# Optimization experiments

Measured on AMD Instinct MI355X. Metric: run time of the kernel, lower is better.

Reference implementation:

```python
import jax, jax.numpy as jnp
import numpy as np

B, N, E = 32, 128, 16384
D, H, O, A = 72, 72, 72, 4   # n_input, n_hidden, n_output, n_node_attr
C_WEIGHT = 1.0
EPS = 1e-5  # BatchNorm1d default eps


def setup_inputs() -> dict:
    key = jax.random.key(0)
    ks = jax.random.split(key, 16)
    rn = lambda k, shp, s=0.05: jax.random.normal(k, shp, jnp.float32) * s
    return {
        "h": jax.random.normal(ks[0], (B, N, D), jnp.float32),
        "x": jax.random.normal(ks[1], (B, N, 4), jnp.float32),
        "edgei": jax.random.randint(ks[2], (B, E), 0, N),
        "edgej": jax.random.randint(ks[3], (B, E), 0, N),
        "node_attr": jax.random.normal(ks[4], (B, N, A), jnp.float32),
        # phi_e: Linear(2D+2 -> H, no bias), BN, ReLU, Linear(H->H), ReLU
        "We1": rn(ks[5], (2 * D + 2, H)),
        "g1": jnp.ones((H,), jnp.float32), "b1": jnp.zeros((H,), jnp.float32),
        "We2": rn(ks[6], (H, H)), "be2": jnp.zeros((H,), jnp.float32),
        # phi_m: Linear(H->1), Sigmoid
        "Wm": rn(ks[7], (H, 1)), "bm": jnp.zeros((1,), jnp.float32),
        # phi_x: Linear(H->H), ReLU, Linear(H->1, no bias, tiny init)
        "Wx1": rn(ks[8], (H, H)), "bx1": jnp.zeros((H,), jnp.float32),
        "Wx2": rn(ks[9], (H, 1), 0.001),
        # phi_h: Linear(H+D+A -> H), BN, ReLU, Linear(H->O)
        "Wh1": rn(ks[10], (H + D + A, H)), "bh1": jnp.zeros((H,), jnp.float32),
        "gh": jnp.ones((H,), jnp.float32), "bh": jnp.zeros((H,), jnp.float32),
        "Wh2": rn(ks[11], (H, O)), "bh2": jnp.zeros((O,), jnp.float32),
    }


def _psi(p):
    return jnp.sign(p) * jnp.log1p(jnp.abs(p))


def _normsq4(p):  # Minkowski norm: p0^2 - p1^2 - p2^2 - p3^2
    psq = p * p
    return 2.0 * psq[..., 0] - psq.sum(axis=-1)


def _dotsq4(p, q):  # Minkowski inner product
    pq = p * q
    return 2.0 * pq[..., 0] - pq.sum(axis=-1)


def _batchnorm(z, g, b):  # training-mode BatchNorm1d over flattened batch dim
    mu = z.mean(axis=0)
    var = z.var(axis=0)
    return (z - mu) * jax.lax.rsqrt(var + EPS) * g + b


_seg_sum = jax.vmap(lambda d, s: jax.ops.segment_sum(d, s, num_segments=N))


def reference(h, x, edgei, edgej, node_attr,
              We1, g1, b1, We2, be2, Wm, bm,
              Wx1, bx1, Wx2, Wh1, bh1, gh, bh, Wh2, bh2):
    # gather edge endpoint features (equiv. to torch.gather along dim 1)
    xi = jnp.take_along_axis(x, edgei[:, :, None], axis=1)    # [B,E,4]
    xj = jnp.take_along_axis(x, edgej[:, :, None], axis=1)
    hi = jnp.take_along_axis(h, edgei[:, :, None], axis=1)    # [B,E,D]
    hj = jnp.take_along_axis(h, edgej[:, :, None], axis=1)
    x_diff = xi - xj
    norms = _psi(_normsq4(x_diff))[..., None]                 # [B,E,1]
    dots = _psi(_dotsq4(xi, xj))[..., None]                   # [B,E,1]

    # m_model: phi_e then sigmoid gate phi_m
    feat = jnp.concatenate([hi, hj, norms, dots], axis=-1)    # [B,E,2D+2]
    z = feat.reshape(-1, 2 * D + 2) @ We1
    z = jax.nn.relu(_batchnorm(z, g1, b1))
    z = jax.nn.relu(z @ We2 + be2)
    m = z.reshape(B, E, H)
    m = m * jax.nn.sigmoid(m @ Wm + bm)                       # gated messages

    # x_model: equivariant coordinate update (segment mean over edges)
    gate = jax.nn.relu(m @ Wx1 + bx1) @ Wx2                   # [B,E,1]
    trans = jnp.clip(x_diff * gate, -100.0, 100.0)
    agg = _seg_sum(trans, edgei)                              # [B,N,4]
    cnt = _seg_sum(jnp.ones_like(trans), edgei)
    x_out = x + (agg / jnp.maximum(cnt, 1.0)) * C_WEIGHT

    # h_model: segment sum of messages, node MLP, residual
    magg = _seg_sum(m, edgei)                                 # [B,N,H]
    hin = jnp.concatenate([h, magg, node_attr], axis=-1).reshape(-1, H + D + A)
    z2 = hin @ Wh1 + bh1
    z2 = jax.nn.relu(_batchnorm(z2, gh, bh))
    z2 = z2 @ Wh2 + bh2
    h_out = h + z2.reshape(B, N, O)

    return (h_out, x_out, m)
```

## Files before the change

kernel.cpp:

```cpp
#include <hip/hip_runtime.h>

#define BB 32
#define NN 128
#define EE 16384
#define ROWS_E (BB*EE)
#define ROWS_N (BB*NN)
#define EPS_BN 1e-5f

#define XOUT_OFF (ROWS_N*72)
#define M_OFF    (XOUT_OFF + ROWS_N*4)

#define ST1_OFF 0
#define ST2_OFF 512
#define AGG_OFF 1024
#define CNT_OFF (AGG_OFF + ROWS_N*4)
#define MAGG_OFF (CNT_OFF + ROWS_N)
#define Z2_OFF (MAGG_OFF + ROWS_N*72)
#define ZERO_FLOATS Z2_OFF
#define WB_OFF (Z2_OFF + ROWS_N*72)

#define WE1T_OFF 0
#define WE2T_OFF 13440
#define WX1T_OFF 21760
#define WH1T_OFF 30080
#define WH2T_OFF 43520
#define WB_TOTAL 51840

typedef __attribute__((ext_vector_type(8))) short short8;
typedef __attribute__((ext_vector_type(4))) float f32x4;

__device__ __forceinline__ float psi_f(float p) {
    return copysignf(log1pf(fabsf(p)), p);
}
__device__ __forceinline__ unsigned short f2bf(float f) {
    union { float f; unsigned u; } v; v.f = f;
    unsigned r = v.u + 0x7fffu + ((v.u >> 16) & 1u);
    return (unsigned short)(r >> 16);
}
__device__ __forceinline__ unsigned pk(float a, float b) {
    return (unsigned)f2bf(a) | ((unsigned)f2bf(b) << 16);
}

__global__ void k_prep(const float* __restrict__ We1, const float* __restrict__ We2,
                       const float* __restrict__ Wx1, const float* __restrict__ Wh1,
                       const float* __restrict__ Wh2, unsigned short* __restrict__ wb)
{
    int idx = blockIdx.x * 256 + threadIdx.x;
    if (idx >= WB_TOTAL) return;
    const float* src; int off, n, k, K;
    if (idx < WE2T_OFF)      { off = idx;            n = off/168; k = off%168; src = We1; K = 146; }
    else if (idx < WH1T_OFF && idx >= WX1T_OFF) { off = idx - WX1T_OFF; n = off/104; k = off%104; src = Wx1; K = 72; }
    else if (idx < WX1T_OFF) { off = idx - WE2T_OFF; n = off/104; k = off%104; src = We2; K = 72; }
    else if (idx < WH2T_OFF) { off = idx - WH1T_OFF; n = off/168; k = off%168; src = Wh1; K = 148; }
    else                     { off = idx - WH2T_OFF; n = off/104; k = off%104; src = Wh2; K = 72; }
    float v = (n < 72 && k < K) ? src[k * 72 + n] : 0.f;
    wb[idx] = f2bf(v);
}

__device__ __forceinline__ void stage_feat(
    unsigned short* At, const float* __restrict__ h, const float* __restrict__ x,
    const int* __restrict__ ei, const int* __restrict__ ej, int tid, int blk)
{
    int rl = tid >> 1, half = tid & 1;
    int row = blk * 128 + rl;
    int b = row >> 14;
    int i = ei[row], j = ej[row];
    int node = half ? j : i;
    const float4* hp = (const float4*)(h + (size_t)(b * 128 + node) * 72);
    uint2* arow = (uint2*)(&At[rl * 160 + half * 72]);
    #pragma unroll
    for (int q = 0; q < 18; q++) {
        float4 v = hp[q];
        arow[q] = make_uint2(pk(v.x, v.y), pk(v.z, v.w));
    }
    if (half == 0) {
        float4 xi = *(const float4*)(x + (size_t)(b * 128 + i) * 4);
        float4 xj = *(const float4*)(x + (size_t)(b * 128 + j) * 4);
        float d0 = xi.x - xj.x, d1 = xi.y - xj.y, d2 = xi.z - xj.z, d3 = xi.w - xj.w;
        float nrm = d0*d0 - d1*d1 - d2*d2 - d3*d3;
        float dot = xi.x*xj.x - xi.y*xj.y - xi.z*xj.z - xi.w*xj.w;
        *(unsigned*)(&At[rl * 160 + 144]) = pk(psi_f(nrm), psi_f(dot));
        unsigned* tp = (unsigned*)(&At[rl * 160 + 146]);
        tp[0] = 0u; tp[1] = 0u; tp[2] = 0u;
    } else {
        unsigned* tp = (unsigned*)(&At[rl * 160 + 152]);
        tp[0] = 0u; tp[1] = 0u; tp[2] = 0u; tp[3] = 0u;
    }
}

__global__ __launch_bounds__(256, 4) void k_edge_stats(
    const float* __restrict__ h, const float* __restrict__ x,
    const int* __restrict__ ei, const int* __restrict__ ej,
    const unsigned short* __restrict__ We1t, float* __restrict__ st)
{
    __shared__ unsigned short At[128 * 160];
    int tid = threadIdx.x;
    stage_feat(At, h, x, ei, ej, tid, blockIdx.x);

    int wv = tid >> 6, lane = tid & 63, c = lane & 15, quad = lane >> 4;
    f32x4 acc[2][5] = {};
    for (int kc = 0; kc < 5; kc++) {
        int k0 = kc * 32 + quad * 8;
        short8 a0 = *(const short8*)(&At[(wv * 32 + c) * 160 + k0]);
        short8 a1 = *(const short8*)(&At[(wv * 32 + 16 + c) * 160 + k0]);
        #pragma unroll
        for (int ct = 0; ct < 5; ct++) {
            short8 bf = *(const short8*)(&We1t[(ct * 16 + c) * 168 + k0]);
            acc[0][ct] = __builtin_amdgcn_mfma_f32_16x16x32_bf16(a0, bf, acc[0][ct], 0, 0, 0);
            acc[1][ct] = __builtin_amdgcn_mfma_f32_16x16x32_bf16(a1, bf, acc[1][ct], 0, 0, 0);
        }
    }
    float* sredw = (float*)(&At[wv * 32 * 160]);
    #pragma unroll
    for (int ct = 0; ct < 5; ct++) {
        int col = ct * 16 + c;
        float s = 0.f, q = 0.f;
        #pragma unroll
        for (int rt = 0; rt < 2; rt++)
            #pragma unroll
            for (int r = 0; r < 4; r++) {
                float v = acc[rt][ct][r];
                s += v; q += v * v;
            }
        s += __shfl_xor(s, 16); s += __shfl_xor(s, 32);
        q += __shfl_xor(q, 16); q += __shfl_xor(q, 32);
        if (lane < 16 && col < 72) { sredw[col] = s; sredw[72 + col] = q; }
    }
    __syncthreads();
    if (tid < 144) {
        const float* a = (const float*)At;
        atomicAdd(&st[tid], a[tid] + a[2560 + tid] + a[5120 + tid] + a[7680 + tid]);
    }
}

__global__ void k_finalize(float* __restrict__ st, float inv_rows)
{
    int c = threadIdx.x;
    if (c < 72) {
        float mean = st[c] * inv_rows;
        float var  = st[72 + c] * inv_rows - mean * mean;
        st[144 + c] = mean;
        st[216 + c] = rsqrtf(var + EPS_BN);
    }
}

__global__ __launch_bounds__(256, 4) void k_edge_fused(
    const float* __restrict__ h, const float* __restrict__ x,
    const int* __restrict__ ei, const int* __restrict__ ej,
    const float* __restrict__ st1, const float* __restrict__ g1, const float* __restrict__ b1,
    const float* __restrict__ be2, const float* __restrict__ Wm, const float* __restrict__ bm,
    const float* __restrict__ bx1, const float* __restrict__ Wx2,
    const unsigned short* __restrict__ We1t, const unsigned short* __restrict__ We2t,
    const unsigned short* __restrict__ Wx1t,
    float* __restrict__ m, float* __restrict__ agg, float* __restrict__ cnt)
{
    __shared__ unsigned short At[128 * 160];
    int tid = threadIdx.x;
    stage_feat(At, h, x, ei, ej, tid, blockIdx.x);

    int wv = tid >> 6, lane = tid & 63, c = lane & 15, quad = lane >> 4;
    f32x4 acc1[2][5] = {};
    for (int kc = 0; kc < 5; kc++) {
        int k0 = kc * 32 + quad * 8;
        short8 a0 = *(const short8*)(&At[(wv * 32 + c) * 160 + k0]);
        short8 a1 = *(const short8*)(&At[(wv * 32 + 16 + c) * 160 + k0]);
        #pragma unroll
        for (int ct = 0; ct < 5; ct++) {
            short8 bf = *(const short8*)(&We1t[(ct * 16 + c) * 168 + k0]);
            acc1[0][ct] = __builtin_amdgcn_mfma_f32_16x16x32_bf16(a0, bf, acc1[0][ct], 0, 0, 0);
            acc1[1][ct] = __builtin_amdgcn_mfma_f32_16x16x32_bf16(a1, bf, acc1[1][ct], 0, 0, 0);
        }
    }
    const float* mean = st1 + 144;
    const float* inv  = st1 + 216;
    #pragma unroll
    for (int ct = 0; ct < 5; ct++) {
        int col = ct * 16 + c;
        float mu = 0.f, iv = 0.f, ga = 0.f, be = 0.f;
        if (col < 72) { mu = mean[col]; iv = inv[col]; ga = g1[col]; be = b1[col]; }
        #pragma unroll
        for (int rt = 0; rt < 2; rt++)
            #pragma unroll
            for (int r = 0; r < 4; r++) {
                float a = (col < 72) ? fmaxf((acc1[rt][ct][r] - mu) * iv * ga + be, 0.f) : 0.f;
                int lrow = wv * 32 + rt * 16 + quad * 4 + r;
                At[lrow * 160 + col] = f2bf(a);
            }
    }
    {
        int r_ = lane >> 1, h_ = lane & 1;
        uint* zp = (uint*)&At[(wv * 32 + r_) * 160 + 80 + h_ * 8];
        zp[0] = 0u; zp[1] = 0u; zp[2] = 0u; zp[3] = 0u;
    }
    f32x4 acc2[2][5] = {};
    for (int kc = 0; kc < 3; kc++) {
        int k0 = kc * 32 + quad * 8;
        short8 a0 = *(const short8*)(&At[(wv * 32 + c) * 160 + k0]);
        short8 a1 = *(const short8*)(&At[(wv * 32 + 16 + c) * 160 + k0]);
        #pragma unroll
        for (int ct = 0; ct < 5; ct++) {
            short8 bf = *(const short8*)(&We2t[(ct * 16 + c) * 104 + k0]);
            acc2[0][ct] = __builtin_amdgcn_mfma_f32_16x16x32_bf16(a0, bf, acc2[0][ct], 0, 0, 0);
            acc2[1][ct] = __builtin_amdgcn_mfma_f32_16x16x32_bf16(a1, bf, acc2[1][ct], 0, 0, 0);
        }
    }
    float part[2][4] = {};
    float bm0 = bm[0];
    #pragma unroll
    for (int ct = 0; ct < 5; ct++) {
        int col = ct * 16 + c;
        float bias = (col < 72) ? be2[col] : 0.f;
        float wm   = (col < 72) ? Wm[col]  : 0.f;
        #pragma unroll
        for (int rt = 0; rt < 2; rt++)
            #pragma unroll
            for (int r = 0; r < 4; r++) {
                float t = fmaxf(acc2[rt][ct][r] + bias, 0.f);
                acc2[rt][ct][r] = t;
                part[rt][r] += t * wm;
            }
    }
    float sg[2][4];
    #pragma unroll
    for (int rt = 0; rt < 2; rt++)
        #pragma unroll
        for (int r = 0; r < 4; r++) {
            float s = part[rt][r];
            s += __shfl_xor(s, 1); s += __shfl_xor(s, 2);
            s += __shfl_xor(s, 4); s += __shfl_xor(s, 8);
            sg[rt][r] = 1.f / (1.f + expf(-(s + bm0)));
        }
    size_t rbase = (size_t)blockIdx.x * 128 + wv * 32 + quad * 4;
    #pragma unroll
    for (int rt = 0; rt < 2; rt++)
        #pragma unroll
        for (int ct = 0; ct < 5; ct++) {
            int col = ct * 16 + c;
            #pragma unroll
            for (int r = 0; r < 4; r++) {
                float mv = acc2[rt][ct][r] * sg[rt][r];
                int lrow = wv * 32 + rt * 16 + quad * 4 + r;
                At[lrow * 160 + col] = f2bf(mv);
                if (col < 72) m[(rbase + rt * 16 + r) * 72 + col] = mv;
            }
        }
    f32x4 acc3[2][5] = {};
    for (int kc = 0; kc < 3; kc++) {
        int k0 = kc * 32 + quad * 8;
        short8 a0 = *(const short8*)(&At[(wv * 32 + c) * 160 + k0]);
        short8 a1 = *(const short8*)(&At[(wv * 32 + 16 + c) * 160 + k0]);
        #pragma unroll
        for (int ct = 0; ct < 5; ct++) {
            short8 bf = *(const short8*)(&Wx1t[(ct * 16 + c) * 104 + k0]);
            acc3[0][ct] = __builtin_amdgcn_mfma_f32_16x16x32_bf16(a0, bf, acc3[0][ct], 0, 0, 0);
            acc3[1][ct] = __builtin_amdgcn_mfma_f32_16x16x32_bf16(a1, bf, acc3[1][ct], 0, 0, 0);
        }
    }
    float part3[2][4] = {};
    #pragma unroll
    for (int ct = 0; ct < 5; ct++) {
        int col = ct * 16 + c;
        float bias = (col < 72) ? bx1[col] : 0.f;
        float wx   = (col < 72) ? Wx2[col] : 0.f;
        #pragma unroll
        for (int rt = 0; rt < 2; rt++)
            #pragma unroll
            for (int r = 0; r < 4; r++)
                part3[rt][r] += fmaxf(acc3[rt][ct][r] + bias, 0.f) * wx;
    }
    float* gp = (float*)&At[(wv * 32) * 160 + 96];
    #pragma unroll
    for (int rt = 0; rt < 2; rt++)
        #pragma unroll
        for (int r = 0; r < 4; r++) {
            float s = part3[rt][r];
            s += __shfl_xor(s, 1); s += __shfl_xor(s, 2);
            s += __shfl_xor(s, 4); s += __shfl_xor(s, 8);
            if (c == 0) gp[rt * 16 + quad * 4 + r] = s;
        }
    __syncthreads();
    if (tid < 128) {
        size_t erow = (size_t)blockIdx.x * 128 + tid;
        int b = (int)(erow >> 14);
        int i2 = ei[erow], j2 = ej[erow];
        float g2 = *((float*)&At[((tid >> 5) * 32) * 160 + 96] + (tid & 31));
        float4 xi = *(const float4*)(x + (size_t)(b * 128 + i2) * 4);
        float4 xj = *(const float4*)(x + (size_t)(b * 128 + j2) * 4);
        float t0 = fminf(fmaxf((xi.x - xj.x) * g2, -100.f), 100.f);
        float t1 = fminf(fmaxf((xi.y - xj.y) * g2, -100.f), 100.f);
        float t2 = fminf(fmaxf((xi.z - xj.z) * g2, -100.f), 100.f);
        float t3 = fminf(fmaxf((xi.w - xj.w) * g2, -100.f), 100.f);
        float* ap = agg + (size_t)(b * 128 + i2) * 4;
        atomicAdd(ap + 0, t0); atomicAdd(ap + 1, t1);
        atomicAdd(ap + 2, t2); atomicAdd(ap + 3, t3);
        atomicAdd(cnt + (size_t)(b * 128 + i2), 1.f);
    }
}

__global__ __launch_bounds__(256, 4) void k_magg(
    const float* __restrict__ m, const int* __restrict__ ei, float* __restrict__ magg)
{
    __shared__ float accum[128 * 72];
    int tid = threadIdx.x;
    for (int q = tid; q < 9216; q += 256) accum[q] = 0.f;
    __syncthreads();
    int b = blockIdx.x >> 3, chunk = blockIdx.x & 7;
    int wv = tid >> 6, lane = tid & 63;
    int ebase = b * 16384 + chunk * 2048;
    for (int e = wv; e < 2048; e += 4) {
        int erow = ebase + e;
        int node = ei[erow];
        const float* mr = m + (size_t)erow * 72;
        atomicAdd(&accum[node * 72 + lane], mr[lane]);
        if (lane < 8) atomicAdd(&accum[node * 72 + 64 + lane], mr[64 + lane]);
    }
    __syncthreads();
    float* mg = magg + (size_t)b * 9216;
    for (int q = tid; q < 9216; q += 256) atomicAdd(&mg[q], accum[q]);
}

__global__ __launch_bounds__(256) void k_node_gemm1(
    const float* __restrict__ h, const float* __restrict__ node_attr,
    const float* __restrict__ magg, const unsigned short* __restrict__ Wh1t,
    const float* __restrict__ bh1, float* __restrict__ z2, float* __restrict__ st)
{
    __shared__ unsigned short At[128 * 168];
    __shared__ unsigned short Wt[80 * 168];
    __shared__ float sred[4][144];
    int tid = threadIdx.x;
    {
        const uint4* s = (const uint4*)Wh1t; uint4* d = (uint4*)Wt;
        for (int q = tid; q < 1680; q += 256) d[q] = s[q];
    }
    int rl = tid >> 1, half = tid & 1;
    size_t row = (size_t)blockIdx.x * 128 + rl;
    const float4* sp = (const float4*)((half ? magg : h) + row * 72);
    uint2* arow = (uint2*)(&At[rl * 168 + half * 72]);
    #pragma unroll
    for (int q = 0; q < 18; q++) {
        float4 v = sp[q];
        arow[q] = make_uint2(pk(v.x, v.y), pk(v.z, v.w));
    }
    if (half) {
        float4 na = *(const float4*)(node_attr + row * 4);
        *(unsigned*)(&At[rl * 168 + 144]) = pk(na.x, na.y);
        *(unsigned*)(&At[rl * 168 + 146]) = pk(na.z, na.w);
        unsigned* tailp = (unsigned*)(&At[rl * 168 + 148]);
        #pragma unroll
        for (int q = 0; q < 10; q++) tailp[q] = 0u;
    }
    __syncthreads();

    int wv = tid >> 6, lane = tid & 63, c = lane & 15, quad = lane >> 4;
    f32x4 acc[2][5] = {};
    for (int kc = 0; kc < 5; kc++) {
        int k0 = kc * 32 + quad * 8;
        short8 a0 = *(const short8*)(&At[(wv * 32 + c) * 168 + k0]);
        short8 a1 = *(const short8*)(&At[(wv * 32 + 16 + c) * 168 + k0]);
        #pragma unroll
        for (int ct = 0; ct < 5; ct++) {
            short8 bf = *(const short8*)(&Wt[(ct * 16 + c) * 168 + k0]);
            acc[0][ct] = __builtin_amdgcn_mfma_f32_16x16x32_bf16(a0, bf, acc[0][ct], 0, 0, 0);
            acc[1][ct] = __builtin_amdgcn_mfma_f32_16x16x32_bf16(a1, bf, acc[1][ct], 0, 0, 0);
        }
    }
    size_t rbase = (size_t)blockIdx.x * 128 + wv * 32 + quad * 4;
    #pragma unroll
    for (int ct = 0; ct < 5; ct++) {
        int col = ct * 16 + c;
        float bias = (col < 72) ? bh1[col] : 0.f;
        float s = 0.f, q = 0.f;
        #pragma unroll
        for (int rt = 0; rt < 2; rt++) {
            float* op = z2 + (rbase + rt * 16) * 72 + col;
            #pragma unroll
            for (int r = 0; r < 4; r++) {
                float v = acc[rt][ct][r] + bias;
                if (col < 72) op[(size_t)r * 72] = v;
                s += v; q += v * v;
            }
        }
        s += __shfl_xor(s, 16); s += __shfl_xor(s, 32);
        q += __shfl_xor(q, 16); q += __shfl_xor(q, 32);
        if (lane < 16 && col < 72) { sred[wv][col] = s; sred[wv][72 + col] = q; }
    }
    __syncthreads();
    if (tid < 144)
        atomicAdd(&st[tid], sred[0][tid] + sred[1][tid] + sred[2][tid] + sred[3][tid]);
}

__global__ __launch_bounds__(256) void k_node_final(
    const float* __restrict__ h, const float* __restrict__ x,
    const float* __restrict__ z2, const float* __restrict__ st2,
    const float* __restrict__ gh, const float* __restrict__ bh,
    const unsigned short* __restrict__ Wh2t, const float* __restrict__ bh2,
    const float* __restrict__ agg, const float* __restrict__ cnt,
    float* __restrict__ hout, float* __restrict__ xout)
{
    __shared__ unsigned short Zt[128 * 104];
    __shared__ unsigned short Wt[80 * 104];
    int tid = threadIdx.x;
    {
        const uint4* s = (const uint4*)Wh2t; uint4* d = (uint4*)Wt;
        for (int q = tid; q < 1040; q += 256) d[q] = s[q];
    }
    int rl = tid >> 1, half = tid & 1;
    size_t row = (size_t)blockIdx.x * 128 + rl;
    const float* mean = st2 + 144;
    const float* inv  = st2 + 216;
    const float4* zp = (const float4*)(z2 + row * 72) + half * 9;
    uint2* arow = (uint2*)(&Zt[rl * 104 + half * 36]);
    #pragma unroll
    for (int q = 0; q < 9; q++) {
        int k = half * 36 + q * 4;
        float4 v = zp[q];
        float a0 = fmaxf((v.x - mean[k  ]) * inv[k  ] * gh[k  ] + bh[k  ], 0.f);
        float a1 = fmaxf((v.y - mean[k+1]) * inv[k+1] * gh[k+1] + bh[k+1], 0.f);
        float a2 = fmaxf((v.z - mean[k+2]) * inv[k+2] * gh[k+2] + bh[k+2], 0.f);
        float a3 = fmaxf((v.w - mean[k+3]) * inv[k+3] * gh[k+3] + bh[k+3], 0.f);
        arow[q] = make_uint2(pk(a0, a1), pk(a2, a3));
    }
    uint2* prow = (uint2*)(&Zt[rl * 104]);
    #pragma unroll
    for (int q = 0; q < 4; q++) prow[18 + half * 4 + q] = make_uint2(0u, 0u);
    __syncthreads();

    int wv = tid >> 6, lane = tid & 63, c = lane & 15, quad = lane >> 4;
    f32x4 acc[2][5] = {};
    for (int kc = 0; kc < 3; kc++) {
        int k0 = kc * 32 + quad * 8;
        short8 a0 = *(const short8*)(&Zt[(wv * 32 + c) * 104 + k0]);
        short8 a1 = *(const short8*)(&Zt[(wv * 32 + 16 + c) * 104 + k0]);
        #pragma unroll
        for (int ct = 0; ct < 5; ct++) {
            short8 bf = *(const short8*)(&Wt[(ct * 16 + c) * 104 + k0]);
            acc[0][ct] = __builtin_amdgcn_mfma_f32_16x16x32_bf16(a0, bf, acc[0][ct], 0, 0, 0);
            acc[1][ct] = __builtin_amdgcn_mfma_f32_16x16x32_bf16(a1, bf, acc[1][ct], 0, 0, 0);
        }
    }
    size_t rbase = (size_t)blockIdx.x * 128 + wv * 32 + quad * 4;
    #pragma unroll
    for (int rt = 0; rt < 2; rt++)
        #pragma unroll
        for (int ct = 0; ct < 5; ct++) {
            int col = ct * 16 + c;
            if (col < 72) {
                float bias = bh2[col];
                #pragma unroll
                for (int r = 0; r < 4; r++) {
                    size_t gr = (rbase + rt * 16 + r);
                    hout[gr * 72 + col] = h[gr * 72 + col] + acc[rt][ct][r] + bias;
                }
            }
        }
    if (tid < 128) {
        size_t nrow = (size_t)blockIdx.x * 128 + tid;
        float cn = fmaxf(cnt[nrow], 1.f);
        float4 ag = *(const float4*)(agg + nrow * 4);
        float4 xv = *(const float4*)(x + nrow * 4);
        ((float4*)xout)[nrow] = make_float4(xv.x + ag.x / cn, xv.y + ag.y / cn,
                                            xv.z + ag.z / cn, xv.w + ag.w / cn);
    }
}

extern "C" void kernel_launch(void* const* d_in, const int* in_sizes, int n_in,
                              void* d_out, int out_size, void* d_ws, size_t ws_size,
                              hipStream_t stream)
{
    const float* h   = (const float*)d_in[0];
    const float* x   = (const float*)d_in[1];
    const int*   ei  = (const int*)d_in[2];
    const int*   ej  = (const int*)d_in[3];
    const float* na  = (const float*)d_in[4];
    const float* We1 = (const float*)d_in[5];
    const float* g1  = (const float*)d_in[6];
    const float* b1  = (const float*)d_in[7];
    const float* We2 = (const float*)d_in[8];
    const float* be2 = (const float*)d_in[9];
    const float* Wm  = (const float*)d_in[10];
    const float* bm  = (const float*)d_in[11];
    const float* Wx1 = (const float*)d_in[12];
    const float* bx1 = (const float*)d_in[13];
    const float* Wx2 = (const float*)d_in[14];
    const float* Wh1 = (const float*)d_in[15];
    const float* bh1 = (const float*)d_in[16];
    const float* gh  = (const float*)d_in[17];
    const float* bhp = (const float*)d_in[18];
    const float* Wh2 = (const float*)d_in[19];
    const float* bh2 = (const float*)d_in[20];

    float* out  = (float*)d_out;
    float* hout = out;
    float* xout = out + XOUT_OFF;
    float* m    = out + M_OFF;
    float* ws   = (float*)d_ws;
    float* st1  = ws + ST1_OFF;
    float* st2  = ws + ST2_OFF;
    float* agg  = ws + AGG_OFF;
    float* cnt  = ws + CNT_OFF;
    float* magg = ws + MAGG_OFF;
    float* z2   = ws + Z2_OFF;
    unsigned short* wb = (unsigned short*)(ws + WB_OFF);

    hipMemsetAsync(d_ws, 0, (size_t)ZERO_FLOATS * sizeof(float), stream);
    k_prep<<<(WB_TOTAL + 255) / 256, 256, 0, stream>>>(We1, We2, Wx1, Wh1, Wh2, wb);
    k_edge_stats<<<ROWS_E / 128, 256, 0, stream>>>(h, x, ei, ej, wb + WE1T_OFF, st1);
    k_finalize<<<1, 128, 0, stream>>>(st1, 1.0f / (float)ROWS_E);
    k_edge_fused<<<ROWS_E / 128, 256, 0, stream>>>(h, x, ei, ej, st1, g1, b1, be2, Wm, bm,
                                                   bx1, Wx2, wb + WE1T_OFF, wb + WE2T_OFF,
                                                   wb + WX1T_OFF, m, agg, cnt);
    k_magg<<<256, 256, 0, stream>>>(m, ei, magg);
    k_node_gemm1<<<ROWS_N / 128, 256, 0, stream>>>(h, na, magg, wb + WH1T_OFF, bh1, z2, st2);
    k_finalize<<<1, 128, 0, stream>>>(st2, 1.0f / (float)ROWS_N);
    k_node_final<<<ROWS_N / 128, 256, 0, stream>>>(h, x, z2, st2, gh, bhp,
                                                   wb + WH2T_OFF, bh2, agg, cnt, hout, xout);
}
```

Before: 680.1 us.

## Fuse message segment-sum into edge kernel via global atomics, pad LDS rows

Removes the separate k_magg kernel. The edge kernel now atomically adds each gated message value directly into the global per-node aggregate, which avoids re-reading the m tensor from memory. The LDS row stride changes from 160 to 168 to reduce bank conflicts, and launch bounds drop from 4 to 3 blocks per SM. The cost is many more global float atomics on only 128 nodes per batch, which can contend heavily, and fewer resident blocks.

After: 766.0 us. 1.13x slower.

```diff
diff --git a/kernel.cpp b/kernel.cpp
--- a/kernel.cpp
+++ b/kernel.cpp
@@ -25,6 +25,8 @@
 #define WH1T_OFF 30080
 #define WH2T_OFF 43520
 #define WB_TOTAL 51840
+
+#define SS 168
 
 typedef __attribute__((ext_vector_type(8))) short short8;
 typedef __attribute__((ext_vector_type(4))) float f32x4;
@@ -67,7 +69,7 @@
     int i = ei[row], j = ej[row];
     int node = half ? j : i;
     const float4* hp = (const float4*)(h + (size_t)(b * 128 + node) * 72);
-    uint2* arow = (uint2*)(&At[rl * 160 + half * 72]);
+    uint2* arow = (uint2*)(&At[rl * SS + half * 72]);
     #pragma unroll
     for (int q = 0; q < 18; q++) {
         float4 v = hp[q];
@@ -79,21 +81,21 @@
         float d0 = xi.x - xj.x, d1 = xi.y - xj.y, d2 = xi.z - xj.z, d3 = xi.w - xj.w;
         float nrm = d0*d0 - d1*d1 - d2*d2 - d3*d3;
         float dot = xi.x*xj.x - xi.y*xj.y - xi.z*xj.z - xi.w*xj.w;
-        *(unsigned*)(&At[rl * 160 + 144]) = pk(psi_f(nrm), psi_f(dot));
-        unsigned* tp = (unsigned*)(&At[rl * 160 + 146]);
+        *(unsigned*)(&At[rl * SS + 144]) = pk(psi_f(nrm), psi_f(dot));
+        unsigned* tp = (unsigned*)(&At[rl * SS + 146]);
         tp[0] = 0u; tp[1] = 0u; tp[2] = 0u;
     } else {
-        unsigned* tp = (unsigned*)(&At[rl * 160 + 152]);
+        unsigned* tp = (unsigned*)(&At[rl * SS + 152]);
         tp[0] = 0u; tp[1] = 0u; tp[2] = 0u; tp[3] = 0u;
     }
 }
 
-__global__ __launch_bounds__(256, 4) void k_edge_stats(
+__global__ __launch_bounds__(256, 3) void k_edge_stats(
     const float* __restrict__ h, const float* __restrict__ x,
     const int* __restrict__ ei, const int* __restrict__ ej,
     const unsigned short* __restrict__ We1t, float* __restrict__ st)
 {
-    __shared__ unsigned short At[128 * 160];
+    __shared__ unsigned short At[128 * SS];
     int tid = threadIdx.x;
     stage_feat(At, h, x, ei, ej, tid, blockIdx.x);
 
@@ -101,8 +103,8 @@
     f32x4 acc[2][5] = {};
     for (int kc = 0; kc < 5; kc++) {
         int k0 = kc * 32 + quad * 8;
-        short8 a0 = *(const short8*)(&At[(wv * 32 + c) * 160 + k0]);
-        short8 a1 = *(const short8*)(&At[(wv * 32 + 16 + c) * 160 + k0]);
+        short8 a0 = *(const short8*)(&At[(wv * 32 + c) * SS + k0]);
+        short8 a1 = *(const short8*)(&At[(wv * 32 + 16 + c) * SS + k0]);
         #pragma unroll
         for (int ct = 0; ct < 5; ct++) {
             short8 bf = *(const short8*)(&We1t[(ct * 16 + c) * 168 + k0]);
@@ -110,7 +112,7 @@
             acc[1][ct] = __builtin_amdgcn_mfma_f32_16x16x32_bf16(a1, bf, acc[1][ct], 0, 0, 0);
         }
     }
-    float* sredw = (float*)(&At[wv * 32 * 160]);
+    float* sredw = (float*)(&At[wv * 32 * SS]);
     #pragma unroll
     for (int ct = 0; ct < 5; ct++) {
         int col = ct * 16 + c;
@@ -129,7 +131,7 @@
     __syncthreads();
     if (tid < 144) {
         const float* a = (const float*)At;
-        atomicAdd(&st[tid], a[tid] + a[2560 + tid] + a[5120 + tid] + a[7680 + tid]);
+        atomicAdd(&st[tid], a[tid] + a[2688 + tid] + a[5376 + tid] + a[8064 + tid]);
     }
 }
 
@@ -144,7 +146,7 @@
     }
 }
 
-__global__ __launch_bounds__(256, 4) void k_edge_fused(
+__global__ __launch_bounds__(256, 3) void k_edge_fused(
     const float* __restrict__ h, const float* __restrict__ x,
     const int* __restrict__ ei, const int* __restrict__ ej,
     const float* __restrict__ st1, const float* __restrict__ g1, const float* __restrict__ b1,
@@ -152,9 +154,10 @@
     const float* __restrict__ bx1, const float* __restrict__ Wx2,
     const unsigned short* __restrict__ We1t, const unsigned short* __restrict__ We2t,
     const unsigned short* __restrict__ Wx1t,
-    float* __restrict__ m, float* __restrict__ agg, float* __restrict__ cnt)
-{
-    __shared__ unsigned short At[128 * 160];
+    float* __restrict__ m, float* __restrict__ agg, float* __restrict__ cnt,
+    float* __restrict__ magg)
+{
+    __shared__ unsigned short At[128 * SS];
     int tid = threadIdx.x;
     stage_feat(At, h, x, ei, ej, tid, blockIdx.x);
 
@@ -162,8 +165,8 @@
     f32x4 acc1[2][5] = {};
     for (int kc = 0; kc < 5; kc++) {
         int k0 = kc * 32 + quad * 8;
-        short8 a0 = *(const short8*)(&At[(wv * 32 + c) * 160 + k0]);
-        short8 a1 = *(const short8*)(&At[(wv * 32 + 16 + c) * 160 + k0]);
+        short8 a0 = *(const short8*)(&At[(wv * 32 + c) * SS + k0]);
+        short8 a1 = *(const short8*)(&At[(wv * 32 + 16 + c) * SS + k0]);
         #pragma unroll
         for (int ct = 0; ct < 5; ct++) {
             short8 bf = *(const short8*)(&We1t[(ct * 16 + c) * 168 + k0]);
@@ -184,19 +187,19 @@
             for (int r = 0; r < 4; r++) {
                 float a = (col < 72) ? fmaxf((acc1[rt][ct][r] - mu) * iv * ga + be, 0.f) : 0.f;
                 int lrow = wv * 32 + rt * 16 + quad * 4 + r;
-                At[lrow * 160 + col] = f2bf(a);
+                At[lrow * SS + col] = f2bf(a);
             }
     }
     {
         int r_ = lane >> 1, h_ = lane & 1;
-        uint* zp = (uint*)&At[(wv * 32 + r_) * 160 + 80 + h_ * 8];
+        uint* zp = (uint*)&At[(wv * 32 + r_) * SS + 80 + h_ * 8];
         zp[0] = 0u; zp[1] = 0u; zp[2] = 0u; zp[3] = 0u;
     }
     f32x4 acc2[2][5] = {};
     for (int kc = 0; kc < 3; kc++) {
         int k0 = kc * 32 + quad * 8;
-        short8 a0 = *(const short8*)(&At[(wv * 32 + c) * 160 + k0]);
-        short8 a1 = *(const short8*)(&At[(wv * 32 + 16 + c) * 160 + k0]);
+        short8 a0 = *(const short8*)(&At[(wv * 32 + c) * SS + k0]);
+        short8 a1 = *(const short8*)(&At[(wv * 32 + 16 + c) * SS + k0]);
         #pragma unroll
         for (int ct = 0; ct < 5; ct++) {
             short8 bf = *(const short8*)(&We2t[(ct * 16 + c) * 104 + k0]);
@@ -231,6 +234,13 @@
             sg[rt][r] = 1.f / (1.f + expf(-(s + bm0)));
         }
     size_t rbase = (size_t)blockIdx.x * 128 + wv * 32 + quad * 4;
+    int bb = blockIdx.x >> 7;
+    int nd[2][4];
+    #pragma unroll
+    for (int rt = 0; rt < 2; rt++)
+        #pragma unroll
+        for (int r = 0; r < 4; r++)
+            nd[rt][r] = ei[rbase + rt * 16 + r];
     #pragma unroll
     for (int rt = 0; rt < 2; rt++)
         #pragma unroll
@@ -240,15 +250,18 @@
             for (int r = 0; r < 4; r++) {
                 float mv = acc2[rt][ct][r] * sg[rt][r];
                 int lrow = wv * 32 + rt * 16 + quad * 4 + r;
-                At[lrow * 160 + col] = f2bf(mv);
-                if (col < 72) m[(rbase + rt * 16 + r) * 72 + col] = mv;
+                At[lrow * SS + col] = f2bf(mv);
+                if (col < 72) {
+                    m[(rbase + rt * 16 + r) * 72 + col] = mv;
+                    atomicAdd(&magg[(size_t)(bb * 128 + nd[rt][r]) * 72 + col], mv);
+                }
             }
         }
     f32x4 acc3[2][5] = {};
     for (int kc = 0; kc < 3; kc++) {
         int k0 = kc * 32 + quad * 8;
-        short8 a0 = *(const short8*)(&At[(wv * 32 + c) * 160 + k0]);
-        short8 a1 = *(const short8*)(&At[(wv * 32 + 16 + c) * 160 + k0]);
+        short8 a0 = *(const short8*)(&At[(wv * 32 + c) * SS + k0]);
+        short8 a1 = *(const short8*)(&At[(wv * 32 + 16 + c) * SS + k0]);
         #pragma unroll
         for (int ct = 0; ct < 5; ct++) {
             short8 bf = *(const short8*)(&Wx1t[(ct * 16 + c) * 104 + k0]);
@@ -268,7 +281,7 @@
             for (int r = 0; r < 4; r++)
                 part3[rt][r] += fmaxf(acc3[rt][ct][r] + bias, 0.f) * wx;
     }
-    float* gp = (float*)&At[(wv * 32) * 160 + 96];
+    float* gp = (float*)&At[(wv * 32) * SS + 96];
     #pragma unroll
     for (int rt = 0; rt < 2; rt++)
         #pragma unroll
@@ -283,7 +296,7 @@
         size_t erow = (size_t)blockIdx.x * 128 + tid;
         int b = (int)(erow >> 14);
         int i2 = ei[erow], j2 = ej[erow];
-        float g2 = *((float*)&At[((tid >> 5) * 32) * 160 + 96] + (tid & 31));
+        float g2 = *((float*)&At[((tid >> 5) * 32) * SS + 96] + (tid & 31));
         float4 xi = *(const float4*)(x + (size_t)(b * 128 + i2) * 4);
         float4 xj = *(const float4*)(x + (size_t)(b * 128 + j2) * 4);
         float t0 = fminf(fmaxf((xi.x - xj.x) * g2, -100.f), 100.f);
@@ -295,28 +308,6 @@
         atomicAdd(ap + 2, t2); atomicAdd(ap + 3, t3);
         atomicAdd(cnt + (size_t)(b * 128 + i2), 1.f);
     }
-}
-
-__global__ __launch_bounds__(256, 4) void k_magg(
-    const float* __restrict__ m, const int* __restrict__ ei, float* __restrict__ magg)
-{
-    __shared__ float accum[128 * 72];
-    int tid = threadIdx.x;
-    for (int q = tid; q < 9216; q += 256) accum[q] = 0.f;
-    __syncthreads();
-    int b = blockIdx.x >> 3, chunk = blockIdx.x & 7;
-    int wv = tid >> 6, lane = tid & 63;
-    int ebase = b * 16384 + chunk * 2048;
-    for (int e = wv; e < 2048; e += 4) {
-        int erow = ebase + e;
-        int node = ei[erow];
-        const float* mr = m + (size_t)erow * 72;
-        atomicAdd(&accum[node * 72 + lane], mr[lane]);
-        if (lane < 8) atomicAdd(&accum[node * 72 + 64 + lane], mr[64 + lane]);
-    }
-    __syncthreads();
-    float* mg = magg + (size_t)b * 9216;
-    for (int q = tid; q < 9216; q += 256) atomicAdd(&mg[q], accum[q]);
 }
 
 __global__ __launch_bounds__(256) void k_node_gemm1(
@@ -508,8 +499,7 @@
     k_finalize<<<1, 128, 0, stream>>>(st1, 1.0f / (float)ROWS_E);
     k_edge_fused<<<ROWS_E / 128, 256, 0, stream>>>(h, x, ei, ej, st1, g1, b1, be2, Wm, bm,
                                                    bx1, Wx2, wb + WE1T_OFF, wb + WE2T_OFF,
-                                                   wb + WX1T_OFF, m, agg, cnt);
-    k_magg<<<256, 256, 0, stream>>>(m, ei, magg);
+                                                   wb + WX1T_OFF, m, agg, cnt, magg);
     k_node_gemm1<<<ROWS_N / 128, 256, 0, stream>>>(h, na, magg, wb + WH1T_OFF, bh1, z2, st2);
     k_finalize<<<1, 128, 0, stream>>>(st2, 1.0f / (float)ROWS_N);
     k_node_final<<<ROWS_N / 128, 256, 0, stream>>>(h, x, z2, st2, gh, bhp,
```
